# Performance work log

Hardware: AMD Instinct MI355X
Metric: run time of the kernel (lower is better)

Reference implementation:

```python
import jax, jax.numpy as jnp
import numpy as np

N = 100000       # nodes
E = 1600000      # edges (avg degree 16)
D_IN = 256
D_HID = 64
D_OUT = 40
PROP_STEP = 16
ALP = 0.5
LAM = 1.0


def setup_inputs() -> dict:
    key = jax.random.key(0)
    ks = jax.random.split(key, 9)
    x = jax.random.normal(ks[0], (N, D_IN), dtype=jnp.float32)
    edge_row = jnp.sort(jax.random.randint(ks[1], (E,), 0, N, dtype=jnp.int32))
    edge_col = jax.random.randint(ks[2], (E,), 0, N, dtype=jnp.int32)
    # normalized-adjacency-like nonnegative values, scaled ~1/deg for stability
    edge_val = jax.random.uniform(ks[3], (E,), dtype=jnp.float32) * (1.0 / 16.0)
    diag_vals = jax.random.uniform(ks[4], (N,), dtype=jnp.float32)
    # MLP params (xavier-normal-ish init, zero bias)
    W1 = jax.random.normal(ks[5], (D_IN, D_HID), dtype=jnp.float32) * np.sqrt(2.0 / (D_IN + D_HID))
    b1 = jnp.zeros((D_HID,), dtype=jnp.float32)
    W2 = jax.random.normal(ks[6], (D_HID, D_OUT), dtype=jnp.float32) * np.sqrt(2.0 / (D_HID + D_OUT))
    b2 = jnp.zeros((D_OUT,), dtype=jnp.float32)
    return {"x": x, "edge_row": edge_row, "edge_col": edge_col,
            "edge_val": edge_val, "diag_vals": diag_vals,
            "W1": W1, "b1": b1, "W2": W2, "b2": b2}


def _spmm(edge_row, edge_col, edge_val, Y):
    # sparse [N,N] @ dense [N,D] via gather + segment-sum
    msgs = edge_val[:, None] * Y[edge_col]          # [E, D]
    return jax.ops.segment_sum(msgs, edge_row, num_segments=N)


def reference(x, edge_row, edge_col, edge_val, diag_vals, W1, b1, W2, b2):
    # mlp_bef: single Linear (num_mlp_before=1, no activation after last layer)
    h = x @ W1 + b1                                  # [N, D_HID]
    # spmm(norm_diag, h) is loop-invariant: norm_diag is diagonal
    src = ALP * diag_vals[:, None] * h               # [N, D_HID]
    Y = h
    for _ in range(PROP_STEP):
        Y = (1.0 - ALP) * Y + (ALP * LAM) * _spmm(edge_row, edge_col, edge_val, Y) + src
    # mlp_aft: init_activate=True -> ReLU (norm='none', dropout=0), then Linear
    Y = jax.nn.relu(Y)
    return Y @ W2 + b2                               # [N, D_OUT]
```

## Files before the change

### kernel.cpp

```cpp
#include <hip/hip_runtime.h>

#define N_NODES 100000
#define N_EDGES 1600000
#define D_IN    256
#define D_HID   64
#define D_OUT   40
#define PROP_N  16

typedef short short8 __attribute__((ext_vector_type(8)));
typedef float f32x4  __attribute__((ext_vector_type(4)));

__device__ __forceinline__ unsigned char f32_to_fp8(float f) {
    int p = __builtin_amdgcn_cvt_pk_fp8_f32(f, f, 0, false);
    return (unsigned char)(p & 0xff);
}
__device__ __forceinline__ unsigned short f32_to_bf16(float f) {
    unsigned int u = __float_as_uint(f);
    unsigned int r = (u + 0x7fffu + ((u >> 16) & 1u)) >> 16;
    return (unsigned short)r;
}
__device__ __forceinline__ unsigned int f32x2_to_bf16x2(float lo, float hi) {
    return (unsigned int)f32_to_bf16(lo) | ((unsigned int)f32_to_bf16(hi) << 16);
}
__device__ __forceinline__ float edge_val(unsigned p) {
    return __uint_as_float((p & 0x7fffu) << 16);
}
__device__ __forceinline__ void fma4(float4& a, float v, unsigned b) {
    a.x = fmaf(v, __builtin_amdgcn_cvt_f32_fp8((int)b, 0), a.x);
    a.y = fmaf(v, __builtin_amdgcn_cvt_f32_fp8((int)b, 1), a.y);
    a.z = fmaf(v, __builtin_amdgcn_cvt_f32_fp8((int)b, 2), a.z);
    a.w = fmaf(v, __builtin_amdgcn_cvt_f32_fp8((int)b, 3), a.w);
}

__global__ __launch_bounds__(256) void build_rowptr(const int* __restrict__ erow,
                                                    int* __restrict__ rp) {
    int r = blockIdx.x * blockDim.x + threadIdx.x;
    if (r > N_NODES) return;
    int lo = 0, hi = N_EDGES;
    while (lo < hi) {
        int mid = (lo + hi) >> 1;
        if (erow[mid] < r) lo = mid + 1; else hi = mid;
    }
    rp[r] = lo;
}

__global__ __launch_bounds__(256) void pack_edges4(const int* __restrict__ ecol,
                                                   const float* __restrict__ evalv,
                                                   unsigned* __restrict__ ep4) {
    int i = blockIdx.x * blockDim.x + threadIdx.x;
    if (i >= N_EDGES) return;
    unsigned bf = f32_to_bf16(evalv[i]);
    ep4[i] = ((unsigned)ecol[i] << 15) | (bf & 0x7fffu);
}

__global__ __launch_bounds__(256) void prep_w1t(const float* __restrict__ W1,
                                                unsigned short* __restrict__ W1T) {
    int i = blockIdx.x * 256 + threadIdx.x;
    if (i >= D_IN * D_HID) return;
    int k = i >> 6, n = i & 63;
    W1T[n * 256 + k] = f32_to_bf16(W1[i]);
}

__global__ __launch_bounds__(64) void mlp1(const float* __restrict__ x,
                                           const unsigned short* __restrict__ W1T,
                                           const float* __restrict__ b1,
                                           const float* __restrict__ diag,
                                           float* __restrict__ Y0f,
                                           unsigned char* __restrict__ Y08,
                                           float* __restrict__ src) {
    const int lane  = threadIdx.x;
    const int l15   = lane & 15;
    const int quad  = lane >> 4;
    const int mbase = blockIdx.x * 16;

    f32x4 acc[4] = {};
    const float* xrow = x + (size_t)(mbase + l15) * D_IN + quad * 8;

    #pragma unroll
    for (int ks = 0; ks < 8; ++ks) {
        float4 f0 = *(const float4*)(xrow + ks * 32);
        float4 f1 = *(const float4*)(xrow + ks * 32 + 4);
        union { short8 v; unsigned int u[4]; } a;
        a.u[0] = f32x2_to_bf16x2(f0.x, f0.y);
        a.u[1] = f32x2_to_bf16x2(f0.z, f0.w);
        a.u[2] = f32x2_to_bf16x2(f1.x, f1.y);
        a.u[3] = f32x2_to_bf16x2(f1.z, f1.w);

        #pragma unroll
        for (int ct = 0; ct < 4; ++ct) {
            short8 b = *(const short8*)(W1T + (ct * 16 + l15) * 256 + ks * 32 + quad * 8);
            acc[ct] = __builtin_amdgcn_mfma_f32_16x16x32_bf16(a.v, b, acc[ct], 0, 0, 0);
        }
    }

    float bias[4];
    #pragma unroll
    for (int ct = 0; ct < 4; ++ct) bias[ct] = b1[ct * 16 + l15];

    #pragma unroll
    for (int reg = 0; reg < 4; ++reg) {
        const int mr = mbase + quad * 4 + reg;
        const float dg = diag[mr];
        #pragma unroll
        for (int ct = 0; ct < 4; ++ct) {
            const int col = ct * 16 + l15;
            const float h = acc[ct][reg] + bias[ct];
            const size_t idx = (size_t)mr * 64 + col;
            Y0f[idx] = h;
            src[idx] = 0.5f * dg * h;
            Y08[idx] = f32_to_fp8(h);
        }
    }
}

__global__ __launch_bounds__(256) void prop_step(const float* __restrict__ Yf,
                                                 const unsigned char* __restrict__ Y8,
                                                 const float* __restrict__ src,
                                                 float* __restrict__ Yof,
                                                 unsigned char* __restrict__ Yo8,
                                                 const int* __restrict__ rp,
                                                 const unsigned* __restrict__ ep4) {
    const int wid  = blockIdx.x * 4 + (threadIdx.x >> 6);
    const int lane = threadIdx.x & 63;
    const int g    = lane >> 4;
    const int fl   = lane & 15;
    const int row  = wid * 4 + g;
    if (row >= N_NODES) return;

    const int e0 = rp[row];
    const int e1 = rp[row + 1];

    const size_t fb = (size_t)row * 64 + fl * 4;
    const float4 yself = *(const float4*)(Yf + fb);
    const float4 sv    = *(const float4*)(src + fb);
    const unsigned char* Y8f = Y8 + fl * 4;

    float4 acc0 = make_float4(0.f, 0.f, 0.f, 0.f);
    float4 acc1 = acc0, acc2 = acc0, acc3 = acc0;

    int e = e0;
    int ea = (e0 + 3) & ~3;
    if (ea > e1) ea = e1;
    for (; e < ea; ++e) {
        unsigned p = ep4[e];
        unsigned b = *(const unsigned*)(Y8f + ((size_t)(p >> 15) << 6));
        fma4(acc0, edge_val(p), b);
    }

    for (; e + 8 <= e1; e += 8) {
        uint4 pa = *(const uint4*)(ep4 + e);
        uint4 pb = *(const uint4*)(ep4 + e + 4);
        unsigned b0 = *(const unsigned*)(Y8f + ((size_t)(pa.x >> 15) << 6));
        unsigned b1 = *(const unsigned*)(Y8f + ((size_t)(pa.y >> 15) << 6));
        unsigned b2 = *(const unsigned*)(Y8f + ((size_t)(pa.z >> 15) << 6));
        unsigned b3 = *(const unsigned*)(Y8f + ((size_t)(pa.w >> 15) << 6));
        unsigned b4 = *(const unsigned*)(Y8f + ((size_t)(pb.x >> 15) << 6));
        unsigned b5 = *(const unsigned*)(Y8f + ((size_t)(pb.y >> 15) << 6));
        unsigned b6 = *(const unsigned*)(Y8f + ((size_t)(pb.z >> 15) << 6));
        unsigned b7 = *(const unsigned*)(Y8f + ((size_t)(pb.w >> 15) << 6));
        fma4(acc0, edge_val(pa.x), b0);
        fma4(acc1, edge_val(pa.y), b1);
        fma4(acc2, edge_val(pa.z), b2);
        fma4(acc3, edge_val(pa.w), b3);
        fma4(acc0, edge_val(pb.x), b4);
        fma4(acc1, edge_val(pb.y), b5);
        fma4(acc2, edge_val(pb.z), b6);
        fma4(acc3, edge_val(pb.w), b7);
    }
    if (e + 4 <= e1) {
        uint4 pa = *(const uint4*)(ep4 + e);
        unsigned b0 = *(const unsigned*)(Y8f + ((size_t)(pa.x >> 15) << 6));
        unsigned b1 = *(const unsigned*)(Y8f + ((size_t)(pa.y >> 15) << 6));
        unsigned b2 = *(const unsigned*)(Y8f + ((size_t)(pa.z >> 15) << 6));
        unsigned b3 = *(const unsigned*)(Y8f + ((size_t)(pa.w >> 15) << 6));
        fma4(acc0, edge_val(pa.x), b0);
        fma4(acc1, edge_val(pa.y), b1);
        fma4(acc2, edge_val(pa.z), b2);
        fma4(acc3, edge_val(pa.w), b3);
        e += 4;
    }
    for (; e < e1; ++e) {
        unsigned p = ep4[e];
        unsigned b = *(const unsigned*)(Y8f + ((size_t)(p >> 15) << 6));
        fma4(acc0, edge_val(p), b);
    }

    float4 accs;
    accs.x = (acc0.x + acc1.x) + (acc2.x + acc3.x);
    accs.y = (acc0.y + acc1.y) + (acc2.y + acc3.y);
    accs.z = (acc0.z + acc1.z) + (acc2.z + acc3.z);
    accs.w = (acc0.w + acc1.w) + (acc2.w + acc3.w);

    float4 o;
    o.x = fmaf(0.5f, yself.x, fmaf(0.5f, accs.x, sv.x));
    o.y = fmaf(0.5f, yself.y, fmaf(0.5f, accs.y, sv.y));
    o.z = fmaf(0.5f, yself.z, fmaf(0.5f, accs.z, sv.z));
    o.w = fmaf(0.5f, yself.w, fmaf(0.5f, accs.w, sv.w));

    *(float4*)(Yof + fb) = o;
    int pk = __builtin_amdgcn_cvt_pk_fp8_f32(o.x, o.y, 0, false);
    pk     = __builtin_amdgcn_cvt_pk_fp8_f32(o.z, o.w, pk, true);
    *(unsigned*)(Yo8 + fb) = (unsigned)pk;
}

__global__ __launch_bounds__(256) void mlp2(const float* __restrict__ Y,
                                            const float* __restrict__ W2,
                                            const float* __restrict__ b2,
                                            float* __restrict__ out) {
    __shared__ float W2s[D_HID * D_OUT];
    __shared__ float b2s[D_OUT];
    int tid = threadIdx.x;
    for (int i = tid; i < D_HID * D_OUT; i += 256) W2s[i] = W2[i];
    if (tid < D_OUT) b2s[tid] = b2[tid];
    __syncthreads();

    int n = blockIdx.x * 256 + tid;
    if (n >= N_NODES) return;

    float acc[D_OUT];
    #pragma unroll
    for (int o = 0; o < D_OUT; ++o) acc[o] = b2s[o];

    const float4* Y4 = (const float4*)(Y + (size_t)n * 64);
    #pragma unroll 4
    for (int k4 = 0; k4 < 16; ++k4) {
        float4 y = Y4[k4];
        float ys[4];
        ys[0] = fmaxf(y.x, 0.0f); ys[1] = fmaxf(y.y, 0.0f);
        ys[2] = fmaxf(y.z, 0.0f); ys[3] = fmaxf(y.w, 0.0f);
        #pragma unroll
        for (int j = 0; j < 4; ++j) {
            int k = k4 * 4 + j;
            #pragma unroll
            for (int o = 0; o < D_OUT; ++o)
                acc[o] = fmaf(ys[j], W2s[k * D_OUT + o], acc[o]);
        }
    }

    float4* o4 = (float4*)(out + (size_t)n * D_OUT);
    #pragma unroll
    for (int q = 0; q < 10; ++q)
        o4[q] = make_float4(acc[4 * q], acc[4 * q + 1], acc[4 * q + 2], acc[4 * q + 3]);
}

extern "C" void kernel_launch(void* const* d_in, const int* in_sizes, int n_in,
                              void* d_out, int out_size, void* d_ws, size_t ws_size,
                              hipStream_t stream) {
    const float* x     = (const float*)d_in[0];
    const int*   erow  = (const int*)  d_in[1];
    const int*   ecol  = (const int*)  d_in[2];
    const float* evalv = (const float*)d_in[3];
    const float* diag  = (const float*)d_in[4];
    const float* W1    = (const float*)d_in[5];
    const float* b1    = (const float*)d_in[6];
    const float* W2    = (const float*)d_in[7];
    const float* b2    = (const float*)d_in[8];
    float* out = (float*)d_out;

    const size_t NV = (size_t)N_NODES * D_HID;
    float*          Y0f = (float*)d_ws;
    float*          Y1f = Y0f + NV;
    float*          src = Y1f + NV;
    unsigned char*  Y08 = (unsigned char*)(src + NV);
    unsigned char*  Y18 = Y08 + NV;
    unsigned*       ep4 = (unsigned*)(Y18 + NV);
    int*            rp  = (int*)(ep4 + N_EDGES);
    unsigned short* W1T = (unsigned short*)
        (((unsigned long long)(rp + N_NODES + 1) + 15ull) & ~15ull);

    build_rowptr<<<(N_NODES + 1 + 255) / 256, 256, 0, stream>>>(erow, rp);
    pack_edges4<<<(N_EDGES + 255) / 256, 256, 0, stream>>>(ecol, evalv, ep4);
    prep_w1t<<<(D_IN * D_HID + 255) / 256, 256, 0, stream>>>(W1, W1T);
    mlp1<<<N_NODES / 16, 64, 0, stream>>>(x, W1T, b1, diag, Y0f, Y08, src);

    float*         Yf[2] = {Y0f, Y1f};
    unsigned char* Y8[2] = {Y08, Y18};
    for (int i = 0; i < PROP_N; ++i) {
        prop_step<<<N_NODES / 16, 256, 0, stream>>>(
            Yf[i & 1], Y8[i & 1], src, Yf[(i + 1) & 1], Y8[(i + 1) & 1], rp, ep4);
    }
    mlp2<<<(N_NODES + 255) / 256, 256, 0, stream>>>(Y0f, W2, b2, out);
}
```

Baseline: 826.2 us.

## Split propagation features into two 32-column fp8 halves and split mlp1 K-loop

The fp8 propagation copy of Y is stored as two separate 32-byte-per-row planes, and each propagation step runs as two kernels that each gather only one half. This shrinks the gather working set per launch so it is more likely to stay cache-resident, at the cost of reading the edge list and row pointers twice per step and doubling launch count. mlp1 also splits its K dimension across two wavefronts, reducing the partial sums through shared memory, to raise parallelism in the first GEMM.

```diff
diff --git a/kernel.cpp b/kernel.cpp
--- a/kernel.cpp
+++ b/kernel.cpp
@@ -61,23 +61,26 @@
     W1T[n * 256 + k] = f32_to_bf16(W1[i]);
 }
 
-__global__ __launch_bounds__(64) void mlp1(const float* __restrict__ x,
-                                           const unsigned short* __restrict__ W1T,
-                                           const float* __restrict__ b1,
-                                           const float* __restrict__ diag,
-                                           float* __restrict__ Y0f,
-                                           unsigned char* __restrict__ Y08,
-                                           float* __restrict__ src) {
-    const int lane  = threadIdx.x;
+__global__ __launch_bounds__(128) void mlp1(const float* __restrict__ x,
+                                            const unsigned short* __restrict__ W1T,
+                                            const float* __restrict__ b1,
+                                            const float* __restrict__ diag,
+                                            float* __restrict__ Y0f,
+                                            unsigned char* __restrict__ Y0a,
+                                            unsigned char* __restrict__ Y0b,
+                                            float* __restrict__ src) {
+    const int tid   = threadIdx.x;
+    const int lane  = tid & 63;
+    const int kh    = tid >> 6;
     const int l15   = lane & 15;
     const int quad  = lane >> 4;
     const int mbase = blockIdx.x * 16;
 
     f32x4 acc[4] = {};
-    const float* xrow = x + (size_t)(mbase + l15) * D_IN + quad * 8;
-
-    #pragma unroll
-    for (int ks = 0; ks < 8; ++ks) {
+    const float* xrow = x + (size_t)(mbase + l15) * D_IN + kh * 128 + quad * 8;
+
+    #pragma unroll
+    for (int ks = 0; ks < 4; ++ks) {
         float4 f0 = *(const float4*)(xrow + ks * 32);
         float4 f1 = *(const float4*)(xrow + ks * 32 + 4);
         union { short8 v; unsigned int u[4]; } a;
@@ -88,10 +91,22 @@
 
         #pragma unroll
         for (int ct = 0; ct < 4; ++ct) {
-            short8 b = *(const short8*)(W1T + (ct * 16 + l15) * 256 + ks * 32 + quad * 8);
+            short8 b = *(const short8*)(W1T + (ct * 16 + l15) * 256 +
+                                        kh * 128 + ks * 32 + quad * 8);
             acc[ct] = __builtin_amdgcn_mfma_f32_16x16x32_bf16(a.v, b, acc[ct], 0, 0, 0);
         }
     }
+
+    __shared__ float red[16][64];
+    if (kh == 1) {
+        #pragma unroll
+        for (int ct = 0; ct < 4; ++ct)
+            #pragma unroll
+            for (int r = 0; r < 4; ++r)
+                red[ct * 4 + r][lane] = acc[ct][r];
+    }
+    __syncthreads();
+    if (kh == 1) return;
 
     float bias[4];
     #pragma unroll
@@ -104,36 +119,38 @@
         #pragma unroll
         for (int ct = 0; ct < 4; ++ct) {
             const int col = ct * 16 + l15;
-            const float h = acc[ct][reg] + bias[ct];
+            const float h = acc[ct][reg] + red[ct * 4 + reg][lane] + bias[ct];
             const size_t idx = (size_t)mr * 64 + col;
             Y0f[idx] = h;
             src[idx] = 0.5f * dg * h;
-            Y08[idx] = f32_to_fp8(h);
+            unsigned char h8 = f32_to_fp8(h);
+            if (col < 32) Y0a[(size_t)mr * 32 + col]        = h8;
+            else          Y0b[(size_t)mr * 32 + (col - 32)] = h8;
         }
     }
 }
 
-__global__ __launch_bounds__(256) void prop_step(const float* __restrict__ Yf,
-                                                 const unsigned char* __restrict__ Y8,
+__global__ __launch_bounds__(256) void prop_half(const float* __restrict__ Yf,
+                                                 const unsigned char* __restrict__ Y8p,
                                                  const float* __restrict__ src,
                                                  float* __restrict__ Yof,
-                                                 unsigned char* __restrict__ Yo8,
+                                                 unsigned char* __restrict__ Yo8p,
                                                  const int* __restrict__ rp,
-                                                 const unsigned* __restrict__ ep4) {
+                                                 const unsigned* __restrict__ ep4,
+                                                 const int foff) {
     const int wid  = blockIdx.x * 4 + (threadIdx.x >> 6);
     const int lane = threadIdx.x & 63;
-    const int g    = lane >> 4;
-    const int fl   = lane & 15;
-    const int row  = wid * 4 + g;
-    if (row >= N_NODES) return;
+    const int g    = lane >> 3;
+    const int fl   = lane & 7;
+    const int row  = wid * 8 + g;
 
     const int e0 = rp[row];
     const int e1 = rp[row + 1];
 
-    const size_t fb = (size_t)row * 64 + fl * 4;
+    const size_t fb = (size_t)row * 64 + foff + fl * 4;
     const float4 yself = *(const float4*)(Yf + fb);
     const float4 sv    = *(const float4*)(src + fb);
-    const unsigned char* Y8f = Y8 + fl * 4;
+    const unsigned char* Y8f = Y8p + fl * 4;
 
     float4 acc0 = make_float4(0.f, 0.f, 0.f, 0.f);
     float4 acc1 = acc0, acc2 = acc0, acc3 = acc0;
@@ -143,45 +160,23 @@
     if (ea > e1) ea = e1;
     for (; e < ea; ++e) {
         unsigned p = ep4[e];
-        unsigned b = *(const unsigned*)(Y8f + ((size_t)(p >> 15) << 6));
+        unsigned b = *(const unsigned*)(Y8f + ((size_t)(p >> 15) << 5));
         fma4(acc0, edge_val(p), b);
     }
-
-    for (; e + 8 <= e1; e += 8) {
+    for (; e + 4 <= e1; e += 4) {
         uint4 pa = *(const uint4*)(ep4 + e);
-        uint4 pb = *(const uint4*)(ep4 + e + 4);
-        unsigned b0 = *(const unsigned*)(Y8f + ((size_t)(pa.x >> 15) << 6));
-        unsigned b1 = *(const unsigned*)(Y8f + ((size_t)(pa.y >> 15) << 6));
-        unsigned b2 = *(const unsigned*)(Y8f + ((size_t)(pa.z >> 15) << 6));
-        unsigned b3 = *(const unsigned*)(Y8f + ((size_t)(pa.w >> 15) << 6));
-        unsigned b4 = *(const unsigned*)(Y8f + ((size_t)(pb.x >> 15) << 6));
-        unsigned b5 = *(const unsigned*)(Y8f + ((size_t)(pb.y >> 15) << 6));
-        unsigned b6 = *(const unsigned*)(Y8f + ((size_t)(pb.z >> 15) << 6));
-        unsigned b7 = *(const unsigned*)(Y8f + ((size_t)(pb.w >> 15) << 6));
+        unsigned b0 = *(const unsigned*)(Y8f + ((size_t)(pa.x >> 15) << 5));
+        unsigned b1 = *(const unsigned*)(Y8f + ((size_t)(pa.y >> 15) << 5));
+        unsigned b2 = *(const unsigned*)(Y8f + ((size_t)(pa.z >> 15) << 5));
+        unsigned b3 = *(const unsigned*)(Y8f + ((size_t)(pa.w >> 15) << 5));
         fma4(acc0, edge_val(pa.x), b0);
         fma4(acc1, edge_val(pa.y), b1);
         fma4(acc2, edge_val(pa.z), b2);
         fma4(acc3, edge_val(pa.w), b3);
-        fma4(acc0, edge_val(pb.x), b4);
-        fma4(acc1, edge_val(pb.y), b5);
-        fma4(acc2, edge_val(pb.z), b6);
-        fma4(acc3, edge_val(pb.w), b7);
-    }
-    if (e + 4 <= e1) {
-        uint4 pa = *(const uint4*)(ep4 + e);
-        unsigned b0 = *(const unsigned*)(Y8f + ((size_t)(pa.x >> 15) << 6));
-        unsigned b1 = *(const unsigned*)(Y8f + ((size_t)(pa.y >> 15) << 6));
-        unsigned b2 = *(const unsigned*)(Y8f + ((size_t)(pa.z >> 15) << 6));
-        unsigned b3 = *(const unsigned*)(Y8f + ((size_t)(pa.w >> 15) << 6));
-        fma4(acc0, edge_val(pa.x), b0);
-        fma4(acc1, edge_val(pa.y), b1);
-        fma4(acc2, edge_val(pa.z), b2);
-        fma4(acc3, edge_val(pa.w), b3);
-        e += 4;
     }
     for (; e < e1; ++e) {
         unsigned p = ep4[e];
-        unsigned b = *(const unsigned*)(Y8f + ((size_t)(p >> 15) << 6));
+        unsigned b = *(const unsigned*)(Y8f + ((size_t)(p >> 15) << 5));
         fma4(acc0, edge_val(p), b);
     }
 
@@ -200,7 +195,7 @@
     *(float4*)(Yof + fb) = o;
     int pk = __builtin_amdgcn_cvt_pk_fp8_f32(o.x, o.y, 0, false);
     pk     = __builtin_amdgcn_cvt_pk_fp8_f32(o.z, o.w, pk, true);
-    *(unsigned*)(Yo8 + fb) = (unsigned)pk;
+    *(unsigned*)(Yo8p + (size_t)row * 32 + fl * 4) = (unsigned)pk;
 }
 
 __global__ __launch_bounds__(256) void mlp2(const float* __restrict__ Y,
@@ -258,12 +253,15 @@
     float* out = (float*)d_out;
 
     const size_t NV = (size_t)N_NODES * D_HID;
+    const size_t NP = (size_t)N_NODES * 32;
     float*          Y0f = (float*)d_ws;
     float*          Y1f = Y0f + NV;
     float*          src = Y1f + NV;
-    unsigned char*  Y08 = (unsigned char*)(src + NV);
-    unsigned char*  Y18 = Y08 + NV;
-    unsigned*       ep4 = (unsigned*)(Y18 + NV);
+    unsigned char*  P0a = (unsigned char*)(src + NV);
+    unsigned char*  P0b = P0a + NP;
+    unsigned char*  P1a = P0b + NP;
+    unsigned char*  P1b = P1a + NP;
+    unsigned*       ep4 = (unsigned*)(P1b + NP);
     int*            rp  = (int*)(ep4 + N_EDGES);
     unsigned short* W1T = (unsigned short*)
         (((unsigned long long)(rp + N_NODES + 1) + 15ull) & ~15ull);
@@ -271,13 +269,17 @@
     build_rowptr<<<(N_NODES + 1 + 255) / 256, 256, 0, stream>>>(erow, rp);
     pack_edges4<<<(N_EDGES + 255) / 256, 256, 0, stream>>>(ecol, evalv, ep4);
     prep_w1t<<<(D_IN * D_HID + 255) / 256, 256, 0, stream>>>(W1, W1T);
-    mlp1<<<N_NODES / 16, 64, 0, stream>>>(x, W1T, b1, diag, Y0f, Y08, src);
+    mlp1<<<N_NODES / 16, 128, 0, stream>>>(x, W1T, b1, diag, Y0f, P0a, P0b, src);
 
     float*         Yf[2] = {Y0f, Y1f};
-    unsigned char* Y8[2] = {Y08, Y18};
+    unsigned char* Pa[2] = {P0a, P1a};
+    unsigned char* Pb[2] = {P0b, P1b};
     for (int i = 0; i < PROP_N; ++i) {
-        prop_step<<<N_NODES / 16, 256, 0, stream>>>(
-            Yf[i & 1], Y8[i & 1], src, Yf[(i + 1) & 1], Y8[(i + 1) & 1], rp, ep4);
+        const int c = i & 1, n = (i + 1) & 1;
+        prop_half<<<N_NODES / 32, 256, 0, stream>>>(
+            Yf[c], Pa[c], src, Yf[n], Pa[n], rp, ep4, 0);
+        prop_half<<<N_NODES / 32, 256, 0, stream>>>(
+            Yf[c], Pb[c], src, Yf[n], Pb[n], rp, ep4, 32);
     }
     mlp2<<<(N_NODES + 255) / 256, 256, 0, stream>>>(Y0f, W2, b2, out);
 }
```

New measurement: 978.5 us. 1.18x slower.
